# Kernel tuning notes

Measured on AMD Instinct MI355X. Metric: run time of the kernel, lower is better.

## Reference

```python
import jax, jax.numpy as jnp
import numpy as np

VOCAB = 77
BLANK = VOCAB          # blank_index=-1 in tf.nn.ctc_greedy_decoder -> last class (77)
PRED_LEN = 30          # ctc_prediction_len


def _greedy_decode_row(best):
    """CTC greedy decode of one row. best: [T] int32 argmax path.
    Collapse consecutive repeats, drop blanks, pad to PRED_LEN with -1
    (matches tf.nn.ctc_greedy_decoder + sparse_to_dense(default=-1))."""
    prev = jnp.concatenate([jnp.full((1,), -1, best.dtype), best[:-1]])
    keep = (best != BLANK) & (best != prev)
    pos = jnp.cumsum(keep.astype(jnp.int32)) - 1
    # route dropped / overflow tokens to a scratch slot PRED_LEN
    pos = jnp.where(keep, jnp.minimum(pos, PRED_LEN), PRED_LEN)
    out = jnp.full((PRED_LEN + 1,), -1, jnp.int32).at[pos].set(best)
    return out[:PRED_LEN]


def setup_inputs() -> dict:
    key = jax.random.key(0)
    k1, k2, k3 = jax.random.split(key, 3)
    B, T, D = 1024, 80, 512
    feat_vec = jax.random.normal(k1, (B, T, D), jnp.float32)
    W = jax.random.normal(k2, (D, VOCAB + 1), jnp.float32) * (1.0 / np.sqrt(D))
    b = jnp.zeros((VOCAB + 1,), jnp.float32)
    y = jax.random.randint(k3, (B, PRED_LEN), 0, VOCAB)
    times = T
    return {"feat_vec": feat_vec, "W": W, "b": b, "y": y, "times": times}


def reference(feat_vec, W, b, y, times):
    # Dense classifier with softmax: [B, T, VOCAB+1]
    logits = jax.nn.softmax(jnp.einsum("btd,dc->btc", feat_vec, W) + b, axis=-1)
    # CTC greedy decode (merge_repeated=True), full sequence length = times = T
    best = jnp.argmax(logits, axis=-1).astype(jnp.int32)  # [B, T]
    res_lab = jax.vmap(_greedy_decode_row)(best)          # [B, PRED_LEN]
    return logits, res_lab
```

## Files before the change

kernel.cpp:

```cpp
#include <hip/hip_runtime.h>
#include <math.h>

#define B_     1024
#define T_     80
#define D_     512
#define C_     78
#define PRED_  30
#define BLANK_ 77
#define NKK    16
#define FRAG   512
#define PLANE_STRIDE (5 * NKK * FRAG)

typedef __attribute__((ext_vector_type(8))) _Float16 f16x8;
typedef __attribute__((ext_vector_type(4))) float    f32x4;

__global__ __launch_bounds__(256) void prep_w(const float* __restrict__ W,
                                              ushort* __restrict__ Wf) {
    int i = blockIdx.x * 256 + threadIdx.x;
    if (i >= 2 * PLANE_STRIDE) return;
    int j    = i & 7;
    int lane = (i >> 3) & 63;
    int kk   = (i >> 9) & 15;
    int rest = i >> 13;
    int ct   = rest % 5;
    int plane = rest / 5;
    int q = lane >> 4, n = lane & 15;
    int k = kk * 32 + q * 8 + j;
    int c = ct * 16 + n;
    float v = (c < C_) ? W[k * C_ + c] : 0.f;
    _Float16 h1 = (_Float16)v;
    union { _Float16 h; ushort u; } cv;
    cv.h = (plane == 0) ? h1 : (_Float16)(v - (float)h1);
    Wf[i] = cv.u;
}

__global__ __launch_bounds__(320, 4) void gemm_ctc(
    const float* __restrict__ feat,
    const ushort* __restrict__ Wf,
    const float* __restrict__ bias,
    float* __restrict__ probs,
    float* __restrict__ lab)
{
    __shared__ int best_s[T_];

    const int tid  = threadIdx.x;
    const int w    = tid >> 6;
    const int lane = tid & 63;
    const int q    = lane >> 4;
    const int n    = lane & 15;

    f32x4 acc[5];
    #pragma unroll
    for (int ct = 0; ct < 5; ++ct)
        acc[ct] = (f32x4){0.f, 0.f, 0.f, 0.f};

    const float*  Ap  = feat + ((size_t)blockIdx.x * T_ + w * 16 + n) * D_ + q * 8;
    const ushort* bp0 = Wf + lane * 8;

    float4 c0 = *(const float4*)(Ap);
    float4 c1 = *(const float4*)(Ap + 4);

    #pragma unroll 2
    for (int kk = 0; kk < NKK; ++kk) {
        const int nk = (kk < NKK - 1) ? kk + 1 : NKK - 1;
        float4 n0 = *(const float4*)(Ap + nk * 32);
        float4 n1 = *(const float4*)(Ap + nk * 32 + 4);

        float v[8] = {c0.x, c0.y, c0.z, c0.w, c1.x, c1.y, c1.z, c1.w};
        f16x8 a1f, a2f;
        #pragma unroll
        for (int j = 0; j < 8; ++j) {
            _Float16 h = (_Float16)v[j];
            a1f[j] = h;
            a2f[j] = (_Float16)(v[j] - (float)h);
        }

        const ushort* bpk = bp0 + kk * FRAG;
        #pragma unroll
        for (int ct = 0; ct < 5; ++ct) {
            const ushort* bp = bpk + ct * (NKK * FRAG);
            f16x8 b1 = *(const f16x8*)bp;
            f16x8 b2 = *(const f16x8*)(bp + PLANE_STRIDE);
            acc[ct] = __builtin_amdgcn_mfma_f32_16x16x32_f16(a1f, b1, acc[ct], 0, 0, 0);
            acc[ct] = __builtin_amdgcn_mfma_f32_16x16x32_f16(a2f, b1, acc[ct], 0, 0, 0);
            acc[ct] = __builtin_amdgcn_mfma_f32_16x16x32_f16(a1f, b2, acc[ct], 0, 0, 0);
        }
        c0 = n0; c1 = n1;
    }

    float x[5][4];
    #pragma unroll
    for (int ct = 0; ct < 5; ++ct) {
        int c = ct * 16 + n;
        bool valid = (c < C_);
        float bv = valid ? bias[c] : 0.f;
        #pragma unroll
        for (int r = 0; r < 4; ++r)
            x[ct][r] = valid ? (acc[ct][r] + bv) : -INFINITY;
    }
    float av[4]; int ai[4];
    #pragma unroll
    for (int r = 0; r < 4; ++r) {
        av[r] = x[0][r]; ai[r] = n;
        #pragma unroll
        for (int ct = 1; ct < 5; ++ct) {
            int c = ct * 16 + n;
            if (x[ct][r] > av[r]) { av[r] = x[ct][r]; ai[r] = c; }
        }
    }
    #pragma unroll
    for (int off = 8; off >= 1; off >>= 1) {
        #pragma unroll
        for (int r = 0; r < 4; ++r) {
            float ov = __shfl_xor(av[r], off, 16);
            int   oi = __shfl_xor(ai[r], off, 16);
            if (ov > av[r] || (ov == av[r] && oi < ai[r])) { av[r] = ov; ai[r] = oi; }
        }
    }
    float s[4] = {0.f, 0.f, 0.f, 0.f};
    #pragma unroll
    for (int ct = 0; ct < 5; ++ct)
        #pragma unroll
        for (int r = 0; r < 4; ++r) {
            x[ct][r] = __expf(x[ct][r] - av[r]);
            s[r] += x[ct][r];
        }
    #pragma unroll
    for (int off = 8; off >= 1; off >>= 1)
        #pragma unroll
        for (int r = 0; r < 4; ++r) s[r] += __shfl_xor(s[r], off, 16);

    const size_t growb = (size_t)blockIdx.x * T_ + w * 16 + q * 4;
    #pragma unroll
    for (int r = 0; r < 4; ++r) {
        float inv = 1.f / s[r];
        float* op = probs + (growb + r) * C_;
        #pragma unroll
        for (int ct = 0; ct < 5; ++ct) {
            int c = ct * 16 + n;
            if (c < C_) __builtin_nontemporal_store(x[ct][r] * inv, op + c);
        }
    }
    if (n == 0) {
        int rl = w * 16 + q * 4;
        #pragma unroll
        for (int r = 0; r < 4; ++r)
            best_s[rl + r] = ai[r];
    }
    __syncthreads();

    if (tid == 0) {
        float* op = lab + (size_t)blockIdx.x * PRED_;
        int prev = -1, pos = 0;
        for (int t2 = 0; t2 < T_; ++t2) {
            int v = best_s[t2];
            if (v != BLANK_ && v != prev) {
                if (pos < PRED_) op[pos] = (float)v;
                ++pos;
            }
            prev = v;
        }
        for (int i2 = (pos < PRED_ ? pos : PRED_); i2 < PRED_; ++i2) op[i2] = -1.f;
    }
}

extern "C" void kernel_launch(void* const* d_in, const int* in_sizes, int n_in,
                              void* d_out, int out_size, void* d_ws, size_t ws_size,
                              hipStream_t stream) {
    const float* feat = (const float*)d_in[0];
    const float* W    = (const float*)d_in[1];
    const float* bias = (const float*)d_in[2];
    float*  probs = (float*)d_out;
    float*  lab   = probs + (size_t)B_ * T_ * C_;
    ushort* Wf    = (ushort*)d_ws;

    hipLaunchKernelGGL(prep_w, dim3(320), dim3(256), 0, stream, W, Wf);
    hipLaunchKernelGGL(gemm_ctc, dim3(B_), dim3(320), 0, stream,
                       feat, Wf, bias, probs, lab);
}
```

Before: 284.5 us.

## Assign column tiles to waves, keep W fragments in registers, cross-wave softmax

Reassigns work so each wave owns one 16-column tile across all 80 time rows, rather than one row tile across all columns. The high-precision W plane for that tile is preloaded into registers and the low plane is streamed two steps ahead. The aim is to stop every wave re-reading all W fragments each k-step. Because each row's classes are now split across waves, softmax and argmax need shared-memory max/sum reductions with an extra barrier. Register pressure also rises, so the launch-bounds occupancy hint drops from 4 to 3.

```diff
diff --git a/kernel.cpp b/kernel.cpp
--- a/kernel.cpp
+++ b/kernel.cpp
@@ -34,14 +34,17 @@
     Wf[i] = cv.u;
 }
 
-__global__ __launch_bounds__(320, 4) void gemm_ctc(
+__global__ __launch_bounds__(320, 3) void gemm_ctc(
     const float* __restrict__ feat,
     const ushort* __restrict__ Wf,
     const float* __restrict__ bias,
     float* __restrict__ probs,
     float* __restrict__ lab)
 {
-    __shared__ int best_s[T_];
+    __shared__ float mxs[5][T_];
+    __shared__ float sms[5][T_];
+    __shared__ int   ais[5][T_];
+    __shared__ int   best_s[T_];
 
     const int tid  = threadIdx.x;
     const int w    = tid >> 6;
@@ -49,105 +52,142 @@
     const int q    = lane >> 4;
     const int n    = lane & 15;
 
+    const ushort* bp1 = Wf + (size_t)(w * NKK) * FRAG + lane * 8;
+    f16x8 b1r[NKK];
+    #pragma unroll
+    for (int kk = 0; kk < NKK; ++kk)
+        b1r[kk] = *(const f16x8*)(bp1 + kk * FRAG);
+
+    const ushort* bp2 = bp1 + PLANE_STRIDE;
+    f16x8 b2a = *(const f16x8*)(bp2);
+    f16x8 b2b = *(const f16x8*)(bp2 + FRAG);
+
+    const float* Ab = feat + ((size_t)blockIdx.x * T_ + n) * D_ + q * 8;
+    float4 bufA[5], bufB[5];
+    #pragma unroll
+    for (int rt = 0; rt < 5; ++rt) {
+        bufA[rt] = *(const float4*)(Ab + rt * 16 * D_);
+        bufB[rt] = *(const float4*)(Ab + rt * 16 * D_ + 4);
+    }
+
     f32x4 acc[5];
     #pragma unroll
-    for (int ct = 0; ct < 5; ++ct)
-        acc[ct] = (f32x4){0.f, 0.f, 0.f, 0.f};
-
-    const float*  Ap  = feat + ((size_t)blockIdx.x * T_ + w * 16 + n) * D_ + q * 8;
-    const ushort* bp0 = Wf + lane * 8;
-
-    float4 c0 = *(const float4*)(Ap);
-    float4 c1 = *(const float4*)(Ap + 4);
-
-    #pragma unroll 2
+    for (int rt = 0; rt < 5; ++rt)
+        acc[rt] = (f32x4){0.f, 0.f, 0.f, 0.f};
+
+    #pragma unroll
     for (int kk = 0; kk < NKK; ++kk) {
-        const int nk = (kk < NKK - 1) ? kk + 1 : NKK - 1;
-        float4 n0 = *(const float4*)(Ap + nk * 32);
-        float4 n1 = *(const float4*)(Ap + nk * 32 + 4);
-
-        float v[8] = {c0.x, c0.y, c0.z, c0.w, c1.x, c1.y, c1.z, c1.w};
-        f16x8 a1f, a2f;
-        #pragma unroll
-        for (int j = 0; j < 8; ++j) {
-            _Float16 h = (_Float16)v[j];
-            a1f[j] = h;
-            a2f[j] = (_Float16)(v[j] - (float)h);
-        }
-
-        const ushort* bpk = bp0 + kk * FRAG;
-        #pragma unroll
-        for (int ct = 0; ct < 5; ++ct) {
-            const ushort* bp = bpk + ct * (NKK * FRAG);
-            f16x8 b1 = *(const f16x8*)bp;
-            f16x8 b2 = *(const f16x8*)(bp + PLANE_STRIDE);
-            acc[ct] = __builtin_amdgcn_mfma_f32_16x16x32_f16(a1f, b1, acc[ct], 0, 0, 0);
-            acc[ct] = __builtin_amdgcn_mfma_f32_16x16x32_f16(a2f, b1, acc[ct], 0, 0, 0);
-            acc[ct] = __builtin_amdgcn_mfma_f32_16x16x32_f16(a1f, b2, acc[ct], 0, 0, 0);
-        }
-        c0 = n0; c1 = n1;
-    }
+        f16x8 b2c = b2a;
+        b2a = b2b;
+        if (kk < NKK - 2) b2b = *(const f16x8*)(bp2 + (kk + 2) * FRAG);
+
+        #pragma unroll
+        for (int rt = 0; rt < 5; ++rt) {
+            float4 f0 = bufA[rt], f1 = bufB[rt];
+            if (kk < NKK - 1) {
+                const float* p = Ab + rt * 16 * D_ + (kk + 1) * 32;
+                bufA[rt] = *(const float4*)(p);
+                bufB[rt] = *(const float4*)(p + 4);
+            }
+            float v[8] = {f0.x, f0.y, f0.z, f0.w, f1.x, f1.y, f1.z, f1.w};
+            f16x8 a1f, a2f;
+            #pragma unroll
+            for (int j = 0; j < 8; ++j) {
+                _Float16 h = (_Float16)v[j];
+                a1f[j] = h;
+                a2f[j] = (_Float16)(v[j] - (float)h);
+            }
+            acc[rt] = __builtin_amdgcn_mfma_f32_16x16x32_f16(a1f, b1r[kk], acc[rt], 0, 0, 0);
+            acc[rt] = __builtin_amdgcn_mfma_f32_16x16x32_f16(a2f, b1r[kk], acc[rt], 0, 0, 0);
+            acc[rt] = __builtin_amdgcn_mfma_f32_16x16x32_f16(a1f, b2c,     acc[rt], 0, 0, 0);
+        }
+    }
+
+    const int  colc   = w * 16 + n;
+    const bool cvalid = (colc < C_);
+    const float bv    = cvalid ? bias[colc] : 0.f;
 
     float x[5][4];
     #pragma unroll
-    for (int ct = 0; ct < 5; ++ct) {
-        int c = ct * 16 + n;
-        bool valid = (c < C_);
-        float bv = valid ? bias[c] : 0.f;
+    for (int rt = 0; rt < 5; ++rt)
         #pragma unroll
         for (int r = 0; r < 4; ++r)
-            x[ct][r] = valid ? (acc[ct][r] + bv) : -INFINITY;
-    }
-    float av[4]; int ai[4];
-    #pragma unroll
-    for (int r = 0; r < 4; ++r) {
-        av[r] = x[0][r]; ai[r] = n;
+            x[rt][r] = cvalid ? (acc[rt][r] + bv) : -INFINITY;
+
+    #pragma unroll
+    for (int rt = 0; rt < 5; ++rt) {
+        float av[4]; int ai[4];
+        #pragma unroll
+        for (int r = 0; r < 4; ++r) { av[r] = x[rt][r]; ai[r] = colc; }
+        #pragma unroll
+        for (int off = 8; off >= 1; off >>= 1) {
+            #pragma unroll
+            for (int r = 0; r < 4; ++r) {
+                float ov = __shfl_xor(av[r], off, 16);
+                int   oi = __shfl_xor(ai[r], off, 16);
+                if (ov > av[r] || (ov == av[r] && oi < ai[r])) { av[r] = ov; ai[r] = oi; }
+            }
+        }
+        if (n == 0) {
+            int row = rt * 16 + q * 4;
+            #pragma unroll
+            for (int r = 0; r < 4; ++r) {
+                mxs[w][row + r] = av[r];
+                ais[w][row + r] = ai[r];
+            }
+        }
+    }
+    __syncthreads();
+
+    if (tid < T_) {
+        float m = mxs[0][tid]; int idx = ais[0][tid];
         #pragma unroll
         for (int ct = 1; ct < 5; ++ct) {
-            int c = ct * 16 + n;
-            if (x[ct][r] > av[r]) { av[r] = x[ct][r]; ai[r] = c; }
-        }
-    }
-    #pragma unroll
-    for (int off = 8; off >= 1; off >>= 1) {
+            float mv = mxs[ct][tid];
+            if (mv > m) { m = mv; idx = ais[ct][tid]; }
+        }
+        best_s[tid] = idx;
+    }
+
+    float e[5][4];
+    #pragma unroll
+    for (int rt = 0; rt < 5; ++rt) {
+        int row = rt * 16 + q * 4;
+        float s[4] = {0.f, 0.f, 0.f, 0.f};
         #pragma unroll
         for (int r = 0; r < 4; ++r) {
-            float ov = __shfl_xor(av[r], off, 16);
-            int   oi = __shfl_xor(ai[r], off, 16);
-            if (ov > av[r] || (ov == av[r] && oi < ai[r])) { av[r] = ov; ai[r] = oi; }
-        }
-    }
-    float s[4] = {0.f, 0.f, 0.f, 0.f};
-    #pragma unroll
-    for (int ct = 0; ct < 5; ++ct)
+            float gm = mxs[0][row + r];
+            #pragma unroll
+            for (int ct = 1; ct < 5; ++ct) gm = fmaxf(gm, mxs[ct][row + r]);
+            e[rt][r] = __expf(x[rt][r] - gm);
+            s[r] = e[rt][r];
+        }
+        #pragma unroll
+        for (int off = 8; off >= 1; off >>= 1)
+            #pragma unroll
+            for (int r = 0; r < 4; ++r) s[r] += __shfl_xor(s[r], off, 16);
+        if (n == 0) {
+            #pragma unroll
+            for (int r = 0; r < 4; ++r) sms[w][row + r] = s[r];
+        }
+    }
+    __syncthreads();
+
+    #pragma unroll
+    for (int rt = 0; rt < 5; ++rt) {
+        int row = rt * 16 + q * 4;
         #pragma unroll
         for (int r = 0; r < 4; ++r) {
-            x[ct][r] = __expf(x[ct][r] - av[r]);
-            s[r] += x[ct][r];
-        }
-    #pragma unroll
-    for (int off = 8; off >= 1; off >>= 1)
-        #pragma unroll
-        for (int r = 0; r < 4; ++r) s[r] += __shfl_xor(s[r], off, 16);
-
-    const size_t growb = (size_t)blockIdx.x * T_ + w * 16 + q * 4;
-    #pragma unroll
-    for (int r = 0; r < 4; ++r) {
-        float inv = 1.f / s[r];
-        float* op = probs + (growb + r) * C_;
-        #pragma unroll
-        for (int ct = 0; ct < 5; ++ct) {
-            int c = ct * 16 + n;
-            if (c < C_) __builtin_nontemporal_store(x[ct][r] * inv, op + c);
-        }
-    }
-    if (n == 0) {
-        int rl = w * 16 + q * 4;
-        #pragma unroll
-        for (int r = 0; r < 4; ++r)
-            best_s[rl + r] = ai[r];
-    }
-    __syncthreads();
+            float tot = sms[0][row + r];
+            #pragma unroll
+            for (int ct = 1; ct < 5; ++ct) tot += sms[ct][row + r];
+            float inv = 1.f / tot;
+            if (cvalid) {
+                float* op = probs + ((size_t)blockIdx.x * T_ + row + r) * C_ + colc;
+                __builtin_nontemporal_store(e[rt][r] * inv, op);
+            }
+        }
+    }
 
     if (tid == 0) {
         float* op = lab + (size_t)blockIdx.x * PRED_;
```

New measurement: 352.8 us. 24.0% more time.

## Stage A tiles via async global-to-LDS loads and split CTC decode into separate kernel

Applied to the files above, without the earlier changes.

The GEMM kernel now processes 64 rows per block with 256 threads. It stages feature tiles into double-buffered, XOR-swizzled LDS using global_load_lds, and register-double-buffers the W fragments under an explicit waitcnt and barrier schedule. This decouples row blocking from sequence boundaries, so the argmax and decode move to a new kernel that rereads the softmax probabilities and recomputes the argmax. The aim is to hide feature-load latency and simplify the epilogue, at the cost of an extra launch and a second read of the probability tensor.

```diff
diff --git a/kernel.cpp b/kernel.cpp
--- a/kernel.cpp
+++ b/kernel.cpp
@@ -10,9 +10,20 @@
 #define NKK    16
 #define FRAG   512
 #define PLANE_STRIDE (5 * NKK * FRAG)
+#define ROWS_PB 64
+#define QBYTES  (ROWS_PB * 512)
 
 typedef __attribute__((ext_vector_type(8))) _Float16 f16x8;
 typedef __attribute__((ext_vector_type(4))) float    f32x4;
+
+#define WAITVM(N) asm volatile("s_waitcnt vmcnt(" #N ")" ::: "memory")
+#define SB __builtin_amdgcn_sched_barrier(0)
+
+__device__ __forceinline__ void load_lds16(const void* g, void* l) {
+    __builtin_amdgcn_global_load_lds(
+        (const __attribute__((address_space(1))) unsigned int*)g,
+        (__attribute__((address_space(3))) unsigned int*)l, 16, 0, 0);
+}
 
 __global__ __launch_bounds__(256) void prep_w(const float* __restrict__ W,
                                               ushort* __restrict__ Wf) {
@@ -34,14 +45,13 @@
     Wf[i] = cv.u;
 }
 
-__global__ __launch_bounds__(320, 4) void gemm_ctc(
+__global__ __launch_bounds__(256) void gemm_ctc(
     const float* __restrict__ feat,
     const ushort* __restrict__ Wf,
     const float* __restrict__ bias,
-    float* __restrict__ probs,
-    float* __restrict__ lab)
+    float* __restrict__ probs)
 {
-    __shared__ int best_s[T_];
+    __shared__ __align__(16) unsigned char Abuf[2][QBYTES];
 
     const int tid  = threadIdx.x;
     const int w    = tid >> 6;
@@ -49,44 +59,90 @@
     const int q    = lane >> 4;
     const int n    = lane & 15;
 
+    const float*  Abase = feat + (size_t)blockIdx.x * ROWS_PB * D_;
+    const ushort* bpL   = Wf + lane * 8;
+
+    auto stageA = [&](int q4) {
+        #pragma unroll
+        for (int l = 0; l < 8; ++l) {
+            int c   = l * 256 + tid;
+            int row = c >> 5;
+            int pos = c & 31;
+            int kl  = pos >> 3;
+            int pc  = pos & 7;
+            const float* g = Abase + (size_t)row * D_ + q4 * 128 + kl * 32
+                                   + (pc ^ (row & 7)) * 4;
+            load_lds16(g, Abuf[q4 & 1] + (size_t)(l * 256 + w * 64) * 16);
+        }
+    };
+
+    f16x8 bE[10], bO[10];
+    #define ISSB(SET, KK) { _Pragma("unroll")                                  \
+        for (int f = 0; f < 10; ++f) {                                         \
+            int pl = f / 5, ct = f % 5;                                        \
+            SET[f] = *(const f16x8*)(bpL + (size_t)pl * PLANE_STRIDE           \
+                                         + (ct * NKK + (KK)) * FRAG); } }
+
     f32x4 acc[5];
     #pragma unroll
     for (int ct = 0; ct < 5; ++ct)
         acc[ct] = (f32x4){0.f, 0.f, 0.f, 0.f};
 
-    const float*  Ap  = feat + ((size_t)blockIdx.x * T_ + w * 16 + n) * D_ + q * 8;
-    const ushort* bp0 = Wf + lane * 8;
-
-    float4 c0 = *(const float4*)(Ap);
-    float4 c1 = *(const float4*)(Ap + 4);
-
-    #pragma unroll 2
-    for (int kk = 0; kk < NKK; ++kk) {
-        const int nk = (kk < NKK - 1) ? kk + 1 : NKK - 1;
-        float4 n0 = *(const float4*)(Ap + nk * 32);
-        float4 n1 = *(const float4*)(Ap + nk * 32 + 4);
-
-        float v[8] = {c0.x, c0.y, c0.z, c0.w, c1.x, c1.y, c1.z, c1.w};
-        f16x8 a1f, a2f;
-        #pragma unroll
-        for (int j = 0; j < 8; ++j) {
-            _Float16 h = (_Float16)v[j];
-            a1f[j] = h;
-            a2f[j] = (_Float16)(v[j] - (float)h);
-        }
-
-        const ushort* bpk = bp0 + kk * FRAG;
-        #pragma unroll
-        for (int ct = 0; ct < 5; ++ct) {
-            const ushort* bp = bpk + ct * (NKK * FRAG);
-            f16x8 b1 = *(const f16x8*)bp;
-            f16x8 b2 = *(const f16x8*)(bp + PLANE_STRIDE);
-            acc[ct] = __builtin_amdgcn_mfma_f32_16x16x32_f16(a1f, b1, acc[ct], 0, 0, 0);
-            acc[ct] = __builtin_amdgcn_mfma_f32_16x16x32_f16(a2f, b1, acc[ct], 0, 0, 0);
-            acc[ct] = __builtin_amdgcn_mfma_f32_16x16x32_f16(a1f, b2, acc[ct], 0, 0, 0);
-        }
-        c0 = n0; c1 = n1;
-    }
+    #define BODY(SET, KK) {                                                    \
+        const float* Ab = (const float*)(Abuf[((KK) >> 2) & 1]);               \
+        int rowl = w * 16 + n;                                                 \
+        int sw   = n & 7;                                                      \
+        float4 f0 = *(const float4*)(Ab + rowl * 128 + ((KK) & 3) * 32         \
+                                        + (((2 * q)     ^ sw) * 4));           \
+        float4 f1 = *(const float4*)(Ab + rowl * 128 + ((KK) & 3) * 32         \
+                                        + (((2 * q + 1) ^ sw) * 4));           \
+        float v[8] = {f0.x, f0.y, f0.z, f0.w, f1.x, f1.y, f1.z, f1.w};         \
+        f16x8 a1f, a2f;                                                        \
+        _Pragma("unroll")                                                      \
+        for (int j = 0; j < 8; ++j) {                                          \
+            _Float16 h = (_Float16)v[j];                                       \
+            a1f[j] = h;                                                        \
+            a2f[j] = (_Float16)(v[j] - (float)h);                              \
+        }                                                                      \
+        _Pragma("unroll")                                                      \
+        for (int ct = 0; ct < 5; ++ct) {                                       \
+            acc[ct] = __builtin_amdgcn_mfma_f32_16x16x32_f16(a1f, SET[ct],     \
+                                                             acc[ct], 0,0,0);  \
+            acc[ct] = __builtin_amdgcn_mfma_f32_16x16x32_f16(a2f, SET[ct],     \
+                                                             acc[ct], 0,0,0);  \
+            acc[ct] = __builtin_amdgcn_mfma_f32_16x16x32_f16(a1f, SET[5+ct],   \
+                                                             acc[ct], 0,0,0);  \
+        } }
+
+    stageA(0); SB; ISSB(bE, 0); SB; ISSB(bO, 1); SB; stageA(1); SB;
+    WAITVM(28);
+    __builtin_amdgcn_s_barrier(); SB;
+    BODY(bE, 0);  SB; ISSB(bE, 2);  SB;
+    BODY(bO, 1);  SB; ISSB(bO, 3);  SB;
+    BODY(bE, 2);  SB; ISSB(bE, 4);  SB;
+    BODY(bO, 3);  SB; ISSB(bO, 5);  SB;
+    WAITVM(20);
+    __builtin_amdgcn_s_barrier(); SB;
+    stageA(2); SB;
+    BODY(bE, 4);  SB; ISSB(bE, 6);  SB;
+    BODY(bO, 5);  SB; ISSB(bO, 7);  SB;
+    BODY(bE, 6);  SB; ISSB(bE, 8);  SB;
+    BODY(bO, 7);  SB; ISSB(bO, 9);  SB;
+    WAITVM(20);
+    __builtin_amdgcn_s_barrier(); SB;
+    stageA(3); SB;
+    BODY(bE, 8);  SB; ISSB(bE, 10); SB;
+    BODY(bO, 9);  SB; ISSB(bO, 11); SB;
+    BODY(bE, 10); SB; ISSB(bE, 12); SB;
+    BODY(bO, 11); SB; ISSB(bO, 13); SB;
+    WAITVM(20);
+    __builtin_amdgcn_s_barrier(); SB;
+    BODY(bE, 12); SB; ISSB(bE, 14); SB;
+    BODY(bO, 13); SB; ISSB(bO, 15); SB;
+    BODY(bE, 14); SB;
+    BODY(bO, 15);
+    #undef BODY
+    #undef ISSB
 
     float x[5][4];
     #pragma unroll
@@ -98,25 +154,17 @@
         for (int r = 0; r < 4; ++r)
             x[ct][r] = valid ? (acc[ct][r] + bv) : -INFINITY;
     }
-    float av[4]; int ai[4];
+    float av[4];
     #pragma unroll
     for (int r = 0; r < 4; ++r) {
-        av[r] = x[0][r]; ai[r] = n;
-        #pragma unroll
-        for (int ct = 1; ct < 5; ++ct) {
-            int c = ct * 16 + n;
-            if (x[ct][r] > av[r]) { av[r] = x[ct][r]; ai[r] = c; }
-        }
-    }
-    #pragma unroll
-    for (int off = 8; off >= 1; off >>= 1) {
-        #pragma unroll
-        for (int r = 0; r < 4; ++r) {
-            float ov = __shfl_xor(av[r], off, 16);
-            int   oi = __shfl_xor(ai[r], off, 16);
-            if (ov > av[r] || (ov == av[r] && oi < ai[r])) { av[r] = ov; ai[r] = oi; }
-        }
-    }
+        av[r] = x[0][r];
+        #pragma unroll
+        for (int ct = 1; ct < 5; ++ct) av[r] = fmaxf(av[r], x[ct][r]);
+    }
+    #pragma unroll
+    for (int off = 8; off >= 1; off >>= 1)
+        #pragma unroll
+        for (int r = 0; r < 4; ++r) av[r] = fmaxf(av[r], __shfl_xor(av[r], off, 16));
     float s[4] = {0.f, 0.f, 0.f, 0.f};
     #pragma unroll
     for (int ct = 0; ct < 5; ++ct)
@@ -130,7 +178,7 @@
         #pragma unroll
         for (int r = 0; r < 4; ++r) s[r] += __shfl_xor(s[r], off, 16);
 
-    const size_t growb = (size_t)blockIdx.x * T_ + w * 16 + q * 4;
+    const size_t growb = (size_t)blockIdx.x * ROWS_PB + w * 16 + q * 4;
     #pragma unroll
     for (int r = 0; r < 4; ++r) {
         float inv = 1.f / s[r];
@@ -141,19 +189,30 @@
             if (c < C_) __builtin_nontemporal_store(x[ct][r] * inv, op + c);
         }
     }
-    if (n == 0) {
-        int rl = w * 16 + q * 4;
-        #pragma unroll
-        for (int r = 0; r < 4; ++r)
-            best_s[rl + r] = ai[r];
+}
+
+__global__ __launch_bounds__(128) void decode_ctc(
+    const float* __restrict__ probs,
+    float* __restrict__ lab)
+{
+    __shared__ int am[T_];
+    const int b = blockIdx.x;
+    const int t = threadIdx.x;
+    if (t < T_) {
+        const float* row = probs + ((size_t)b * T_ + t) * C_;
+        float m = row[0]; int idx = 0;
+        for (int c = 1; c < C_; ++c) {
+            float v = row[c];
+            if (v > m) { m = v; idx = c; }
+        }
+        am[t] = idx;
     }
     __syncthreads();
-
-    if (tid == 0) {
-        float* op = lab + (size_t)blockIdx.x * PRED_;
+    if (t == 0) {
+        float* op = lab + (size_t)b * PRED_;
         int prev = -1, pos = 0;
         for (int t2 = 0; t2 < T_; ++t2) {
-            int v = best_s[t2];
+            int v = am[t2];
             if (v != BLANK_ && v != prev) {
                 if (pos < PRED_) op[pos] = (float)v;
                 ++pos;
@@ -175,6 +234,7 @@
     ushort* Wf    = (ushort*)d_ws;
 
     hipLaunchKernelGGL(prep_w, dim3(320), dim3(256), 0, stream, W, Wf);
-    hipLaunchKernelGGL(gemm_ctc, dim3(B_), dim3(320), 0, stream,
-                       feat, Wf, bias, probs, lab);
-}
+    hipLaunchKernelGGL(gemm_ctc, dim3(B_ * T_ / ROWS_PB), dim3(256), 0, stream,
+                       feat, Wf, bias, probs);
+    hipLaunchKernelGGL(decode_ctc, dim3(B_), dim3(128), 0, stream, probs, lab);
+}
```

New measurement: 270.3 us. -5.0%, faster.

## Stage A and W tiles through LDS with async double-buffered global_load_lds

Applied to the files above, without the earlier changes.

Each block now processes two batch rows (160 rows) with 640 threads. Feature and split-fp16 weight fragments are staged into LDS through direct global-to-LDS loads, using a swizzled layout, double buffering and explicit vmcnt waits and barriers. This lets global loads of the next K slab overlap the MFMA work, and each block shares one weight copy across ten waves instead of every wave fetching weights from global memory. The cost is about 120KB of LDS per block, which limits occupancy, plus hand-written wait counts that depend on the exact number of issued loads.

```diff
diff --git a/kernel.cpp b/kernel.cpp
--- a/kernel.cpp
+++ b/kernel.cpp
@@ -10,9 +10,21 @@
 #define NKK    16
 #define FRAG   512
 #define PLANE_STRIDE (5 * NKK * FRAG)
+#define ROWS_PB 160
+#define A_SL   40960
+#define B_SL   20480
 
 typedef __attribute__((ext_vector_type(8))) _Float16 f16x8;
 typedef __attribute__((ext_vector_type(4))) float    f32x4;
+
+#define WAITVM(N) asm volatile("s_waitcnt vmcnt(" #N ")" ::: "memory")
+#define SB __builtin_amdgcn_sched_barrier(0)
+
+__device__ __forceinline__ void load_lds16(const void* g, void* l) {
+    __builtin_amdgcn_global_load_lds(
+        (const __attribute__((address_space(1))) unsigned int*)g,
+        (__attribute__((address_space(3))) unsigned int*)l, 16, 0, 0);
+}
 
 __global__ __launch_bounds__(256) void prep_w(const float* __restrict__ W,
                                               ushort* __restrict__ Wf) {
@@ -34,14 +46,16 @@
     Wf[i] = cv.u;
 }
 
-__global__ __launch_bounds__(320, 4) void gemm_ctc(
+__global__ __launch_bounds__(640) void gemm_ctc(
     const float* __restrict__ feat,
     const ushort* __restrict__ Wf,
     const float* __restrict__ bias,
     float* __restrict__ probs,
     float* __restrict__ lab)
 {
-    __shared__ int best_s[T_];
+    __shared__ __align__(16) unsigned char Abuf[2][A_SL];
+    __shared__ __align__(16) unsigned char Bbuf[2][B_SL];
+    __shared__ int best_s[2][T_];
 
     const int tid  = threadIdx.x;
     const int w    = tid >> 6;
@@ -49,44 +63,86 @@
     const int q    = lane >> 4;
     const int n    = lane & 15;
 
+    const float* Abase = feat + (size_t)blockIdx.x * ROWS_PB * D_;
+
+    auto bundle = [&](int e) {
+        unsigned char* Ad = Abuf[e & 1];
+        unsigned char* Bd = Bbuf[e & 1];
+        #pragma unroll
+        for (int l = 0; l < 4; ++l) {
+            int c   = l * 640 + tid;
+            int row = c >> 4;
+            int pos = c & 15;
+            int kl  = pos >> 3;
+            int pc  = pos & 7;
+            const float* g = Abase + (size_t)row * D_ + e * 64 + kl * 32
+                                   + (pc ^ (row & 7)) * 4;
+            load_lds16(g, Ad + (size_t)(l * 640 + w * 64) * 16);
+        }
+        #pragma unroll
+        for (int i = 0; i < 2; ++i) {
+            int s  = w * 2 + i;
+            int p  = (s >= 10) ? 1 : 0;
+            int s2 = s - p * 10;
+            int ct = s2 >> 1;
+            int kl = s2 & 1;
+            const ushort* g = Wf + (size_t)p * PLANE_STRIDE
+                                 + (ct * NKK + 2 * e + kl) * FRAG + lane * 8;
+            load_lds16(g, Bd + (size_t)s * 1024);
+        }
+    };
+
     f32x4 acc[5];
     #pragma unroll
     for (int ct = 0; ct < 5; ++ct)
         acc[ct] = (f32x4){0.f, 0.f, 0.f, 0.f};
 
-    const float*  Ap  = feat + ((size_t)blockIdx.x * T_ + w * 16 + n) * D_ + q * 8;
-    const ushort* bp0 = Wf + lane * 8;
-
-    float4 c0 = *(const float4*)(Ap);
-    float4 c1 = *(const float4*)(Ap + 4);
-
-    #pragma unroll 2
-    for (int kk = 0; kk < NKK; ++kk) {
-        const int nk = (kk < NKK - 1) ? kk + 1 : NKK - 1;
-        float4 n0 = *(const float4*)(Ap + nk * 32);
-        float4 n1 = *(const float4*)(Ap + nk * 32 + 4);
-
-        float v[8] = {c0.x, c0.y, c0.z, c0.w, c1.x, c1.y, c1.z, c1.w};
-        f16x8 a1f, a2f;
-        #pragma unroll
-        for (int j = 0; j < 8; ++j) {
-            _Float16 h = (_Float16)v[j];
-            a1f[j] = h;
-            a2f[j] = (_Float16)(v[j] - (float)h);
-        }
-
-        const ushort* bpk = bp0 + kk * FRAG;
-        #pragma unroll
-        for (int ct = 0; ct < 5; ++ct) {
-            const ushort* bp = bpk + ct * (NKK * FRAG);
-            f16x8 b1 = *(const f16x8*)bp;
-            f16x8 b2 = *(const f16x8*)(bp + PLANE_STRIDE);
-            acc[ct] = __builtin_amdgcn_mfma_f32_16x16x32_f16(a1f, b1, acc[ct], 0, 0, 0);
-            acc[ct] = __builtin_amdgcn_mfma_f32_16x16x32_f16(a2f, b1, acc[ct], 0, 0, 0);
-            acc[ct] = __builtin_amdgcn_mfma_f32_16x16x32_f16(a1f, b2, acc[ct], 0, 0, 0);
-        }
-        c0 = n0; c1 = n1;
-    }
+    #define BODY(KK) {                                                         \
+        const float*  Ab = (const float*)(Abuf[((KK) >> 1) & 1]);              \
+        const ushort* Bb = (const ushort*)(Bbuf[((KK) >> 1) & 1]);             \
+        const int kl  = (KK) & 1;                                              \
+        int rowl = w * 16 + n;                                                 \
+        int sw   = n & 7;                  \
+        float4 f0 = *(const float4*)(Ab + rowl * 64 + kl * 32                  \
+                                        + (((2 * q)     ^ sw) * 4));           \
+        float4 f1 = *(const float4*)(Ab + rowl * 64 + kl * 32                  \
+                                        + (((2 * q + 1) ^ sw) * 4));           \
+        float v[8] = {f0.x, f0.y, f0.z, f0.w, f1.x, f1.y, f1.z, f1.w};         \
+        f16x8 a1f, a2f;                                                        \
+        _Pragma("unroll")                                                      \
+        for (int j = 0; j < 8; ++j) {                                          \
+            _Float16 h = (_Float16)v[j];                                       \
+            a1f[j] = h;                                                        \
+            a2f[j] = (_Float16)(v[j] - (float)h);                              \
+        }                                                                      \
+        _Pragma("unroll")                                                      \
+        for (int ct = 0; ct < 5; ++ct) {                                       \
+            f16x8 b1 = *(const f16x8*)(Bb + (ct * 2 + kl) * 512 + lane * 8);   \
+            f16x8 b2 = *(const f16x8*)(Bb + (10 + ct * 2 + kl) * 512 + lane * 8);\
+            acc[ct] = __builtin_amdgcn_mfma_f32_16x16x32_f16(a1f, b1,          \
+                                                             acc[ct], 0,0,0);  \
+            acc[ct] = __builtin_amdgcn_mfma_f32_16x16x32_f16(a2f, b1,          \
+                                                             acc[ct], 0,0,0);  \
+            acc[ct] = __builtin_amdgcn_mfma_f32_16x16x32_f16(a1f, b2,          \
+                                                             acc[ct], 0,0,0);  \
+        } }
+
+    bundle(0); SB;
+    bundle(1); SB;
+
+    #define PH(E, NW)                                                          \
+        WAITVM(NW);                                                            \
+        __builtin_amdgcn_s_barrier(); SB;                                      \
+        BODY(2 * (E));                                                         \
+        BODY(2 * (E) + 1);                                                     \
+        SB;                                                                    \
+        __builtin_amdgcn_s_barrier(); SB;                                      \
+        if ((E) <= 5) { bundle((E) + 2); SB; }
+
+    PH(0, 6) PH(1, 6) PH(2, 6) PH(3, 6)
+    PH(4, 6) PH(5, 6) PH(6, 6) PH(7, 0)
+    #undef PH
+    #undef BODY
 
     float x[5][4];
     #pragma unroll
@@ -130,7 +186,7 @@
         #pragma unroll
         for (int r = 0; r < 4; ++r) s[r] += __shfl_xor(s[r], off, 16);
 
-    const size_t growb = (size_t)blockIdx.x * T_ + w * 16 + q * 4;
+    const size_t growb = (size_t)blockIdx.x * ROWS_PB + w * 16 + q * 4;
     #pragma unroll
     for (int r = 0; r < 4; ++r) {
         float inv = 1.f / s[r];
@@ -144,16 +200,19 @@
     if (n == 0) {
         int rl = w * 16 + q * 4;
         #pragma unroll
-        for (int r = 0; r < 4; ++r)
-            best_s[rl + r] = ai[r];
+        for (int r = 0; r < 4; ++r) {
+            int rr = rl + r;
+            best_s[rr / T_][rr % T_] = ai[r];
+        }
     }
     __syncthreads();
 
-    if (tid == 0) {
-        float* op = lab + (size_t)blockIdx.x * PRED_;
+    if (tid < 2) {
+        const int* bs = best_s[tid];
+        float* op = lab + ((size_t)blockIdx.x * 2 + tid) * PRED_;
         int prev = -1, pos = 0;
         for (int t2 = 0; t2 < T_; ++t2) {
-            int v = best_s[t2];
+            int v = bs[t2];
             if (v != BLANK_ && v != prev) {
                 if (pos < PRED_) op[pos] = (float)v;
                 ++pos;
@@ -175,6 +234,6 @@
     ushort* Wf    = (ushort*)d_ws;
 
     hipLaunchKernelGGL(prep_w, dim3(320), dim3(256), 0, stream, W, Wf);
-    hipLaunchKernelGGL(gemm_ctc, dim3(B_), dim3(320), 0, stream,
+    hipLaunchKernelGGL(gemm_ctc, dim3(B_ * T_ / ROWS_PB), dim3(640), 0, stream,
                        feat, Wf, bias, probs, lab);
 }
```

After: 262.8 us. 7.6% less time.
